# Performance work log

Measured on AMD Instinct MI355X. Metric: run time of the kernel, lower is better.

Reference implementation:

```python
import jax, jax.numpy as jnp
import numpy as np

N, H, E, P = 100000, 64, 1600000, 3


def setup_inputs() -> dict:
    key = jax.random.key(0)
    ks = jax.random.split(key, 12)
    h = jax.random.normal(ks[0], (N, H), dtype=jnp.float32)
    W = jax.random.normal(ks[1], (P, H, H), dtype=jnp.float32) * 0.1
    b = jnp.zeros((P, H), dtype=jnp.float32)
    a = jnp.full((P,), 0.25, dtype=jnp.float32)  # PReLU slopes (torch default init)
    fc_w = jax.random.normal(ks[2], (H, H), dtype=jnp.float32) * 0.1
    fc_b = jnp.zeros((H,), dtype=jnp.float32)
    att = jax.random.normal(ks[3], (H,), dtype=jnp.float32) * 0.1
    adj_vals = jax.random.uniform(ks[4], (E,), dtype=jnp.float32) * (1.0 / 16.0)
    row = jax.random.randint(ks[5], (E,), 0, N, dtype=jnp.int32)
    col = jax.random.randint(ks[6], (E,), 0, N, dtype=jnp.int32)
    mask1 = jax.random.randint(ks[7], (N,), 0, 2, dtype=jnp.int32).astype(bool)
    mask2 = jax.random.randint(ks[8], (N,), 0, 2, dtype=jnp.int32).astype(bool)
    return {"h": h, "W": W, "b": b, "a": a, "fc_w": fc_w, "fc_b": fc_b,
            "att": att, "adj_vals": adj_vals, "row": row, "col": col,
            "mask1": mask1, "mask2": mask2}


def reference(h, W, b, a, fc_w, fc_b, att, adj_vals, row, col, mask1, mask2):
    n = h.shape[0]

    def gcn_all(x):
        # P GCN layers (small fixed P): linear -> spmm(adj) -> +bias -> PReLU
        outs = []
        for p in range(W.shape[0]):
            fts = x @ W[p].T                                   # [N,H]
            msg = fts[col] * adj_vals[:, None]                  # [E,H] gather
            agg = jax.ops.segment_sum(msg, row, num_segments=n) # [N,H] scatter-add
            o = agg + b[p]
            outs.append(jnp.where(o > 0, o, a[p] * o))          # PReLU
        return jnp.stack(outs)                                  # [P,N,H]

    def attention(embeds):
        # sp_p = mean_n tanh(fc(embed_p)); beta = softmax_p(att . sp_p)
        s = jnp.tanh(jnp.einsum('pnh,kh->pnk', embeds, fc_w) + fc_b).mean(axis=1)  # [P,H]
        beta = jax.nn.softmax(s @ att, axis=0)                                      # [P]
        return jnp.einsum('pnh,p->nh', embeds, beta)                                # [N,H]

    h_masked = h * (~mask1)[:, None].astype(h.dtype)
    z_mp = attention(gcn_all(h_masked))       # encode with mask_ratio1
    z_mp2 = attention(gcn_all(h))             # encode with mask_ratio 0
    z_masked = z_mp * (~mask2)[:, None].astype(h.dtype)
    x_recon = attention(gcn_all(z_masked))    # decode
    return (z_mp, z_mp2, x_recon)
```

## Files before the change

kernel.cpp:

```cpp
#include <hip/hip_runtime.h>
#include <hip/hip_bf16.h>

typedef __hip_bfloat16 bf16;
typedef __attribute__((ext_vector_type(8))) short bf16x8;
typedef __attribute__((ext_vector_type(4))) float f32x4;


__device__ __forceinline__ short f2bf(float x) {
    unsigned u = __float_as_uint(x);
    unsigned r = (u + 0x7FFFu + ((u >> 16) & 1u)) >> 16;
    return (short)r;
}
__device__ __forceinline__ float bf2f(short s) {
    return __uint_as_float(((unsigned)(unsigned short)s) << 16);
}
__device__ __forceinline__ void split1(float v, short& h, short& l) {
    h = f2bf(v);
    l = f2bf(v - bf2f(h));
}

__device__ __forceinline__ void split8(const float* __restrict__ p, bool ok, bf16x8& hi,
                                       bf16x8& lo) {
    float v[8];
    if (ok) {
        float4 x0 = ((const float4*)p)[0];
        float4 x1 = ((const float4*)p)[1];
        v[0] = x0.x; v[1] = x0.y; v[2] = x0.z; v[3] = x0.w;
        v[4] = x1.x; v[5] = x1.y; v[6] = x1.z; v[7] = x1.w;
    } else {
#pragma unroll
        for (int j = 0; j < 8; j++) v[j] = 0.f;
    }
#pragma unroll
    for (int j = 0; j < 8; j++) {
        short hb = f2bf(v[j]);
        hi[j] = hb;
        lo[j] = f2bf(v[j] - bf2f(hb));
    }
}

__device__ __forceinline__ float fast_tanh(float x) {
    x = fminf(fmaxf(x, -15.f), 15.f);
    float t = __expf(2.f * x);
    return __fdividef(t - 1.f, t + 1.f);
}

__device__ __forceinline__ void fma4(float4& acc, float v, const float4& x) {
    acc.x = fmaf(v, x.x, acc.x);
    acc.y = fmaf(v, x.y, acc.y);
    acc.z = fmaf(v, x.z, acc.z);
    acc.w = fmaf(v, x.w, acc.w);
}

__device__ __forceinline__ void red4(float4& a) {
    a.x += __shfl_xor(a.x, 16); a.y += __shfl_xor(a.y, 16);
    a.z += __shfl_xor(a.z, 16); a.w += __shfl_xor(a.w, 16);
    a.x += __shfl_xor(a.x, 32); a.y += __shfl_xor(a.y, 32);
    a.z += __shfl_xor(a.z, 32); a.w += __shfl_xor(a.w, 32);
}

__global__ __launch_bounds__(256) void forensic_kernel(const unsigned int* __restrict__ mask_w,
                                                       const unsigned int* __restrict__ idx_w,
                                                       int nw_mask, int nw_idx,
                                                       int* __restrict__ flags) {
    __shared__ int sm[6];
    int t = threadIdx.x;
    if (t < 6) sm[t] = 0;
    __syncthreads();
    int m_gt1 = 0, m_f32 = 0, m_f64 = 0, m_oddnz = 0, i_hi = 0, i_oddnz = 0;
    for (int i = t; i < nw_mask; i += 256) {
        unsigned int w = mask_w[i];
        if (w > 1u && w != 0x3F800000u && w != 0x3FF00000u) m_gt1++;
        if (w == 0x3F800000u) m_f32++;
        if ((i & 1) && w == 0x3FF00000u) m_f64++;
        if ((i & 1) && w != 0u) m_oddnz++;
    }
    for (int i = t; i < nw_idx; i += 256) {
        unsigned int v = idx_w[i];
        if (v >= 0x20000000u) i_hi++;
        if ((i & 1) && v != 0u) i_oddnz++;
    }
    atomicAdd(&sm[0], m_gt1);
    atomicAdd(&sm[1], m_f32);
    atomicAdd(&sm[2], m_f64);
    atomicAdd(&sm[3], m_oddnz);
    atomicAdd(&sm[4], i_hi);
    atomicAdd(&sm[5], i_oddnz);
    __syncthreads();
    if (t == 0) {
        int mmode;
        if (sm[1] > 50) mmode = 2;
        else if (sm[2] > 50) mmode = 4;
        else if (sm[0] > 50) mmode = 0;
        else if (sm[3] > 50) mmode = 1;
        else mmode = 3;
        int imode;
        if (sm[4] > (nw_idx * 3) / 4) imode = 2;
        else if (sm[4] > nw_idx / 4) imode = 4;
        else if (sm[5] > 50) imode = 1;
        else imode = 3;
        flags[0] = mmode;
        flags[1] = imode;
    }
}

__device__ __forceinline__ int fetch_idx(const void* p, int e, int mode) {
    switch (mode) {
        case 1: return ((const int*)p)[e];
        case 3: return (int)(((const long long*)p)[e]);
        case 2: return (int)(((const float*)p)[e]);
        default: return (int)(((const double*)p)[e]);
    }
}

__device__ __forceinline__ bool conv_one(const void* m, int mode, int i) {
    switch (mode) {
        case 0: return ((const unsigned char*)m)[i] != 0;
        case 1: return ((const int*)m)[i] != 0;
        case 2: return ((const float*)m)[i] != 0.f;
        case 3: return ((const long long*)m)[i] != 0;
        default: return ((const double*)m)[i] != 0.0;
    }
}

__global__ __launch_bounds__(256) void conv_masks(const void* __restrict__ m1,
                                                  const void* __restrict__ m2,
                                                  const int* __restrict__ flags, int n,
                                                  unsigned char* __restrict__ o1,
                                                  unsigned char* __restrict__ o2) {
    int mode = flags[0];
    int i = blockIdx.x * 256 + threadIdx.x;
    if (i >= n) return;
    o1[i] = conv_one(m1, mode, i) ? 1 : 0;
    o2[i] = conv_one(m2, mode, i) ? 1 : 0;
}


__global__ __launch_bounds__(256) void bucket_hist(const void* __restrict__ row,
                                                   const int* __restrict__ flags, int e_cnt,
                                                   int n, int shift, int nb,
                                                   int* __restrict__ bcnt) {
    __shared__ int hist[2048];
    int t = threadIdx.x;
    for (int i = t; i < nb; i += 256) hist[i] = 0;
    __syncthreads();
    int imode = flags[1];
    for (int e = blockIdx.x * 256 + t; e < e_cnt; e += gridDim.x * 256) {
        int r = fetch_idx(row, e, imode);
        if ((unsigned)r < (unsigned)n) atomicAdd(&hist[r >> shift], 1);
    }
    __syncthreads();
    for (int i = t; i < nb; i += 256)
        if (hist[i]) atomicAdd(&bcnt[i], hist[i]);
}

__global__ __launch_bounds__(1024) void bucket_scan(int* __restrict__ bptr, int nb,
                                                    int* __restrict__ bcur, int n,
                                                    int* __restrict__ row_ptr) {
    __shared__ int sh[1024];
    int t = threadIdx.x;
    int i0 = t * 2, i1 = t * 2 + 1;
    int a = (i0 < nb) ? bptr[i0] : 0;
    int b = (i1 < nb) ? bptr[i1] : 0;
    int s = a + b;
    sh[t] = s;
    __syncthreads();
    for (int off = 1; off < 1024; off <<= 1) {
        int u = (t >= off) ? sh[t - off] : 0;
        __syncthreads();
        sh[t] += u;
        __syncthreads();
    }
    int base = sh[t] - s;
    if (i0 < nb) { bptr[i0] = base; bcur[i0] = base; }
    if (i1 < nb) { bptr[i1] = base + a; bcur[i1] = base + a; }
    if (t == 1023) {
        bptr[nb] = sh[1023];
        row_ptr[n] = sh[1023];
    }
}

__global__ __launch_bounds__(256) void bin_pass2(const void* __restrict__ row,
                                                 const void* __restrict__ col,
                                                 const float* __restrict__ vals,
                                                 const int* __restrict__ flags, int e_cnt, int n,
                                                 int shift, int nb, int* __restrict__ bcur,
                                                 int2* __restrict__ rcbin,
                                                 float* __restrict__ valbin) {
    __shared__ int hist[2048];
    __shared__ int base[2048];
    int t = threadIdx.x;
    int e0 = blockIdx.x * 2048;
    if (e0 >= e_cnt) return;
    int imode = flags[1];
    for (int i = t; i < nb; i += 256) hist[i] = 0;
    __syncthreads();
    int rr[8], cc[8];
    float vv[8];
    bool ok[8];
#pragma unroll
    for (int j = 0; j < 8; j++) {
        int e = e0 + j * 256 + t;
        ok[j] = false;
        if (e < e_cnt) {
            int r = fetch_idx(row, e, imode);
            if ((unsigned)r < (unsigned)n) {
                ok[j] = true;
                rr[j] = r;
                int c = fetch_idx(col, e, imode);
                cc[j] = ((unsigned)c < (unsigned)n) ? c : 0;
                vv[j] = vals[e];
                atomicAdd(&hist[r >> shift], 1);
            }
        }
    }
    __syncthreads();
    for (int i = t; i < nb; i += 256) {
        int c = hist[i];
        base[i] = c ? atomicAdd(&bcur[i], c) : 0;
        hist[i] = 0;
    }
    __syncthreads();
#pragma unroll
    for (int j = 0; j < 8; j++) {
        if (ok[j]) {
            int bk = rr[j] >> shift;
            int pos = base[bk] + atomicAdd(&hist[bk], 1);
            rcbin[pos] = make_int2(rr[j], cc[j]);
            valbin[pos] = vv[j];
        }
    }
}

__global__ __launch_bounds__(512) void csr_finalize(const int* __restrict__ bptr,
                                                    const int2* __restrict__ rcbin,
                                                    const float* __restrict__ valbin, int n,
                                                    int shift, int* __restrict__ row_ptr,
                                                    int* __restrict__ col_s,
                                                    float* __restrict__ val_s) {
    __shared__ int cnt[1024];
    __shared__ int curs[1024];
    __shared__ int red[512];
    int b = blockIdx.x, t = threadIdx.x;
    int rpb = 1 << shift;
    int r0 = b << shift;
    int rows = n - r0;
    if (rows <= 0) return;
    if (rows > rpb) rows = rpb;
    int ebase = bptr[b], eend = bptr[b + 1];
    for (int i = t; i < rows; i += 512) cnt[i] = 0;
    __syncthreads();
    for (int e = ebase + t; e < eend; e += 512) atomicAdd(&cnt[rcbin[e].x - r0], 1);
    __syncthreads();
    int v[2], s = 0;
#pragma unroll
    for (int j = 0; j < 2; j++) {
        int idx = t * 2 + j;
        v[j] = (idx < rows) ? cnt[idx] : 0;
        s += v[j];
    }
    red[t] = s;
    __syncthreads();
    for (int off = 1; off < 512; off <<= 1) {
        int u = (t >= off) ? red[t - off] : 0;
        __syncthreads();
        red[t] += u;
        __syncthreads();
    }
    int run = ebase + red[t] - s;
#pragma unroll
    for (int j = 0; j < 2; j++) {
        int idx = t * 2 + j;
        if (idx < rows) {
            row_ptr[r0 + idx] = run;
            curs[idx] = run;
            run += v[j];
        }
    }
    __syncthreads();
    for (int e = ebase + t; e < eend; e += 512) {
        int2 rc = rcbin[e];
        float vv = valbin[e];
        int pos = atomicAdd(&curs[rc.x - r0], 1);
        col_s[pos] = rc.y;
        val_s[pos] = vv;
    }
}


__device__ __forceinline__ void store_split4(short* __restrict__ hi, short* __restrict__ lo,
                                             size_t o, const float4& v) {
    short4 h4, l4;
    split1(v.x, h4.x, l4.x); split1(v.y, h4.y, l4.y);
    split1(v.z, h4.z, l4.z); split1(v.w, h4.w, l4.w);
    *(short4*)(hi + o) = h4;
    *(short4*)(lo + o) = l4;
}

__global__ __launch_bounds__(256) void spmm_dual(const float* __restrict__ X,
                                                 const int* __restrict__ row_ptr,
                                                 const int* __restrict__ col_s,
                                                 const float* __restrict__ val_s,
                                                 const unsigned char* __restrict__ mask, int n,
                                                 short* __restrict__ axm_hi,
                                                 short* __restrict__ axm_lo,
                                                 short* __restrict__ axf_hi,
                                                 short* __restrict__ axf_lo) {
    int gid = blockIdx.x * 256 + threadIdx.x;
    int r = gid >> 6;
    if (r >= n) return;
    int lane = threadIdx.x & 63;
    int g = lane >> 4, sub = lane & 15;
    int s = row_ptr[r], e = row_ptr[r + 1];
    int cnt = e - s;
    int myc = 0;
    float myvf = 0.f, myvm = 0.f;
    if (lane < cnt) {
        myc = col_s[s + lane];
        float v = val_s[s + lane];
        myvf = v;
        myvm = mask[myc] ? 0.f : v;
    }
    int cmain = cnt > 64 ? 64 : cnt;
    float4 fA = {0, 0, 0, 0}, fB = {0, 0, 0, 0}, mA = {0, 0, 0, 0}, mB = {0, 0, 0, 0};
    for (int i = 0; i < cmain; i += 16) {
        int i0 = i + g, i1 = i + 4 + g, i2 = i + 8 + g, i3 = i + 12 + g;
        int c0 = __shfl(myc, i0), c1 = __shfl(myc, i1);
        int c2 = __shfl(myc, i2), c3 = __shfl(myc, i3);
        float vf0 = __shfl(myvf, i0), vf1 = __shfl(myvf, i1);
        float vf2 = __shfl(myvf, i2), vf3 = __shfl(myvf, i3);
        float vm0 = __shfl(myvm, i0), vm1 = __shfl(myvm, i1);
        float vm2 = __shfl(myvm, i2), vm3 = __shfl(myvm, i3);
        if (i0 < cmain) {
            float4 x = *(const float4*)(X + (size_t)c0 * 64 + sub * 4);
            fma4(fA, vf0, x);
            fma4(mA, vm0, x);
        }
        if (i1 < cmain) {
            float4 x = *(const float4*)(X + (size_t)c1 * 64 + sub * 4);
            fma4(fB, vf1, x);
            fma4(mB, vm1, x);
        }
        if (i2 < cmain) {
            float4 x = *(const float4*)(X + (size_t)c2 * 64 + sub * 4);
            fma4(fA, vf2, x);
            fma4(mA, vm2, x);
        }
        if (i3 < cmain) {
            float4 x = *(const float4*)(X + (size_t)c3 * 64 + sub * 4);
            fma4(fB, vf3, x);
            fma4(mB, vm3, x);
        }
    }
    for (int i = 64 + g; i < cnt; i += 4) {
        int c = col_s[s + i];
        float v = val_s[s + i];
        float vm = mask[c] ? 0.f : v;
        float4 x = *(const float4*)(X + (size_t)c * 64 + sub * 4);
        fma4(fA, v, x);
        fma4(mA, vm, x);
    }
    fA.x += fB.x; fA.y += fB.y; fA.z += fB.z; fA.w += fB.w;
    mA.x += mB.x; mA.y += mB.y; mA.z += mB.z; mA.w += mB.w;
    red4(fA);
    red4(mA);
    if (g == 0) {
        size_t o = (size_t)r * 64 + sub * 4;
        store_split4(axf_hi, axf_lo, o, fA);
        store_split4(axm_hi, axm_lo, o, mA);
    }
}

__global__ __launch_bounds__(256) void spmm_one(const float* __restrict__ X,
                                                const int* __restrict__ row_ptr,
                                                const int* __restrict__ col_s,
                                                const float* __restrict__ val_s,
                                                const unsigned char* __restrict__ mask, int n,
                                                short* __restrict__ ax_hi,
                                                short* __restrict__ ax_lo) {
    int gid = blockIdx.x * 256 + threadIdx.x;
    int r = gid >> 6;
    if (r >= n) return;
    int lane = threadIdx.x & 63;
    int g = lane >> 4, sub = lane & 15;
    int s = row_ptr[r], e = row_ptr[r + 1];
    int cnt = e - s;
    int myc = 0;
    float myv = 0.f;
    if (lane < cnt) {
        myc = col_s[s + lane];
        float v = val_s[s + lane];
        myv = mask[myc] ? 0.f : v;
    }
    int cmain = cnt > 64 ? 64 : cnt;
    float4 aA = {0, 0, 0, 0}, aB = {0, 0, 0, 0};
    for (int i = 0; i < cmain; i += 16) {
        int i0 = i + g, i1 = i + 4 + g, i2 = i + 8 + g, i3 = i + 12 + g;
        int c0 = __shfl(myc, i0), c1 = __shfl(myc, i1);
        int c2 = __shfl(myc, i2), c3 = __shfl(myc, i3);
        float v0 = __shfl(myv, i0), v1 = __shfl(myv, i1);
        float v2 = __shfl(myv, i2), v3 = __shfl(myv, i3);
        if (i0 < cmain && v0 != 0.f) {
            float4 x = *(const float4*)(X + (size_t)c0 * 64 + sub * 4);
            fma4(aA, v0, x);
        }
        if (i1 < cmain && v1 != 0.f) {
            float4 x = *(const float4*)(X + (size_t)c1 * 64 + sub * 4);
            fma4(aB, v1, x);
        }
        if (i2 < cmain && v2 != 0.f) {
            float4 x = *(const float4*)(X + (size_t)c2 * 64 + sub * 4);
            fma4(aA, v2, x);
        }
        if (i3 < cmain && v3 != 0.f) {
            float4 x = *(const float4*)(X + (size_t)c3 * 64 + sub * 4);
            fma4(aB, v3, x);
        }
    }
    for (int i = 64 + g; i < cnt; i += 4) {
        int c = col_s[s + i];
        if (mask[c]) continue;
        float v = val_s[s + i];
        float4 x = *(const float4*)(X + (size_t)c * 64 + sub * 4);
        fma4(aA, v, x);
    }
    aA.x += aB.x; aA.y += aB.y; aA.z += aB.z; aA.w += aB.w;
    red4(aA);
    if (g == 0) {
        size_t o = (size_t)r * 64 + sub * 4;
        store_split4(ax_hi, ax_lo, o, aA);
    }
}


template <int PP>
__global__ __launch_bounds__(256) void gemm_tanh(const short* __restrict__ Xhi0,
                                                 const short* __restrict__ Xlo0,
                                                 const short* __restrict__ Xhi1,
                                                 const short* __restrict__ Xlo1,
                                                 const float* __restrict__ Wg,
                                                 const float* __restrict__ b,
                                                 const float* __restrict__ a,
                                                 const float* __restrict__ fcw,
                                                 const float* __restrict__ fcb, int n, int ntiles,
                                                 float* __restrict__ s_sums) {
    __shared__ __align__(16) short ehi[PP][16][72], elo[PP][16][72];
    int set = blockIdx.y;
    const short* __restrict__ Xhi = set ? Xhi1 : Xhi0;
    const short* __restrict__ Xlo = set ? Xlo1 : Xlo0;
    float* __restrict__ ss = s_sums + set * 512;
    int t = threadIdx.x;
    int wv = t >> 6, lane = t & 63, nl = lane & 15, q = lane >> 4;
    int colg = wv * 16 + nl;
    bf16x8 whi[PP][2], wlo[PP][2];
    float bias[PP], slope[PP];
#pragma unroll
    for (int p = 0; p < PP; p++) {
#pragma unroll
        for (int kk = 0; kk < 2; kk++)
            split8(Wg + p * 4096 + colg * 64 + kk * 32 + q * 8, true, whi[p][kk], wlo[p][kk]);
        bias[p] = b[p * 64 + colg];
        slope[p] = a[p];
    }
    bf16x8 fhi[2], flo[2];
#pragma unroll
    for (int kk = 0; kk < 2; kk++)
        split8(fcw + colg * 64 + kk * 32 + q * 8, true, fhi[kk], flo[kk]);
    float fbias = fcb[colg];
    float ssum[PP];
#pragma unroll
    for (int p = 0; p < PP; p++) ssum[p] = 0.f;

    int rt = blockIdx.x;
    bf16x8 ah[2], al[2];
    if (rt < ntiles) {
        size_t rb = (size_t)(rt * 16 + nl) * 64 + q * 8;
#pragma unroll
        for (int kk = 0; kk < 2; kk++) {
            ah[kk] = *(const bf16x8*)(Xhi + rb + kk * 32);
            al[kk] = *(const bf16x8*)(Xlo + rb + kk * 32);
        }
    }
    for (; rt < ntiles; rt += gridDim.x) {
#pragma unroll
        for (int p = 0; p < PP; p++) {
            f32x4 acc = {0.f, 0.f, 0.f, 0.f};
            acc = __builtin_amdgcn_mfma_f32_16x16x32_bf16(ah[0], whi[p][0], acc, 0, 0, 0);
            acc = __builtin_amdgcn_mfma_f32_16x16x32_bf16(ah[1], whi[p][1], acc, 0, 0, 0);
            acc = __builtin_amdgcn_mfma_f32_16x16x32_bf16(al[0], whi[p][0], acc, 0, 0, 0);
            acc = __builtin_amdgcn_mfma_f32_16x16x32_bf16(al[1], whi[p][1], acc, 0, 0, 0);
            acc = __builtin_amdgcn_mfma_f32_16x16x32_bf16(ah[0], wlo[p][0], acc, 0, 0, 0);
            acc = __builtin_amdgcn_mfma_f32_16x16x32_bf16(ah[1], wlo[p][1], acc, 0, 0, 0);
            acc = __builtin_amdgcn_mfma_f32_16x16x32_bf16(al[0], wlo[p][0], acc, 0, 0, 0);
            acc = __builtin_amdgcn_mfma_f32_16x16x32_bf16(al[1], wlo[p][1], acc, 0, 0, 0);
#pragma unroll
            for (int i = 0; i < 4; i++) {
                float o = acc[i] + bias[p];
                o = (o > 0.f) ? o : slope[p] * o;
                short hb, lb;
                split1(o, hb, lb);
                ehi[p][q * 4 + i][colg] = hb;
                elo[p][q * 4 + i][colg] = lb;
            }
        }
        int rn = rt + gridDim.x;
        bf16x8 pfh[2], pfl[2];
        if (rn < ntiles) {
            size_t rb = (size_t)(rn * 16 + nl) * 64 + q * 8;
#pragma unroll
            for (int kk = 0; kk < 2; kk++) {
                pfh[kk] = *(const bf16x8*)(Xhi + rb + kk * 32);
                pfl[kk] = *(const bf16x8*)(Xlo + rb + kk * 32);
            }
        }
        __syncthreads();
#pragma unroll
        for (int p = 0; p < PP; p++) {
            bf16x8 eh[2], el[2];
#pragma unroll
            for (int kk = 0; kk < 2; kk++) {
                eh[kk] = *(const bf16x8*)(&ehi[p][nl][kk * 32 + q * 8]);
                el[kk] = *(const bf16x8*)(&elo[p][nl][kk * 32 + q * 8]);
            }
            f32x4 acc = {0.f, 0.f, 0.f, 0.f};
            acc = __builtin_amdgcn_mfma_f32_16x16x32_bf16(eh[0], fhi[0], acc, 0, 0, 0);
            acc = __builtin_amdgcn_mfma_f32_16x16x32_bf16(eh[1], fhi[1], acc, 0, 0, 0);
            acc = __builtin_amdgcn_mfma_f32_16x16x32_bf16(el[0], fhi[0], acc, 0, 0, 0);
            acc = __builtin_amdgcn_mfma_f32_16x16x32_bf16(el[1], fhi[1], acc, 0, 0, 0);
            acc = __builtin_amdgcn_mfma_f32_16x16x32_bf16(eh[0], flo[0], acc, 0, 0, 0);
            acc = __builtin_amdgcn_mfma_f32_16x16x32_bf16(eh[1], flo[1], acc, 0, 0, 0);
#pragma unroll
            for (int i = 0; i < 4; i++) {
                int r = rt * 16 + q * 4 + i;
                if (r < n) ssum[p] += fast_tanh(acc[i] + fbias);
            }
        }
        __syncthreads();
#pragma unroll
        for (int kk = 0; kk < 2; kk++) {
            ah[kk] = pfh[kk];
            al[kk] = pfl[kk];
        }
    }
#pragma unroll
    for (int p = 0; p < PP; p++) {
        float s = ssum[p];
        s += __shfl_xor(s, 16);
        s += __shfl_xor(s, 32);
        if (q == 0) atomicAdd(&ss[p * 64 + colg], s);
    }
}


template <int PP>
__global__ __launch_bounds__(256) void gemm_mix(const short* __restrict__ Xhi0,
                                                const short* __restrict__ Xlo0,
                                                const short* __restrict__ Xhi1,
                                                const short* __restrict__ Xlo1,
                                                const float* __restrict__ Wg,
                                                const float* __restrict__ b,
                                                const float* __restrict__ a,
                                                const float* __restrict__ beta, int n, int ntiles,
                                                float* __restrict__ outbase, int accum) {
    int set = blockIdx.y;
    const short* __restrict__ Xhi = set ? Xhi1 : Xhi0;
    const short* __restrict__ Xlo = set ? Xlo1 : Xlo0;
    float* __restrict__ out = outbase + (size_t)set * n * 64;
    int t = threadIdx.x;
    int wv = t >> 6, lane = t & 63, nl = lane & 15, q = lane >> 4;
    int colg = wv * 16 + nl;
    bf16x8 whi[PP][2], wlo[PP][2];
    float bias[PP], slope[PP], bet[PP];
#pragma unroll
    for (int p = 0; p < PP; p++) {
#pragma unroll
        for (int kk = 0; kk < 2; kk++)
            split8(Wg + p * 4096 + colg * 64 + kk * 32 + q * 8, true, whi[p][kk], wlo[p][kk]);
        bias[p] = b[p * 64 + colg];
        slope[p] = a[p];
        bet[p] = beta[set * 8 + p];
    }
    int rt = blockIdx.x;
    bf16x8 ah[2], al[2];
    if (rt < ntiles) {
        size_t rb = (size_t)(rt * 16 + nl) * 64 + q * 8;
#pragma unroll
        for (int kk = 0; kk < 2; kk++) {
            ah[kk] = *(const bf16x8*)(Xhi + rb + kk * 32);
            al[kk] = *(const bf16x8*)(Xlo + rb + kk * 32);
        }
    }
    for (; rt < ntiles; rt += gridDim.x) {
        int rn = rt + gridDim.x;
        bf16x8 pfh[2], pfl[2];
        if (rn < ntiles) {
            size_t rb = (size_t)(rn * 16 + nl) * 64 + q * 8;
#pragma unroll
            for (int kk = 0; kk < 2; kk++) {
                pfh[kk] = *(const bf16x8*)(Xhi + rb + kk * 32);
                pfl[kk] = *(const bf16x8*)(Xlo + rb + kk * 32);
            }
        }
        float mix[4] = {0.f, 0.f, 0.f, 0.f};
#pragma unroll
        for (int p = 0; p < PP; p++) {
            f32x4 acc = {0.f, 0.f, 0.f, 0.f};
            acc = __builtin_amdgcn_mfma_f32_16x16x32_bf16(ah[0], whi[p][0], acc, 0, 0, 0);
            acc = __builtin_amdgcn_mfma_f32_16x16x32_bf16(ah[1], whi[p][1], acc, 0, 0, 0);
            acc = __builtin_amdgcn_mfma_f32_16x16x32_bf16(al[0], whi[p][0], acc, 0, 0, 0);
            acc = __builtin_amdgcn_mfma_f32_16x16x32_bf16(al[1], whi[p][1], acc, 0, 0, 0);
            acc = __builtin_amdgcn_mfma_f32_16x16x32_bf16(ah[0], wlo[p][0], acc, 0, 0, 0);
            acc = __builtin_amdgcn_mfma_f32_16x16x32_bf16(ah[1], wlo[p][1], acc, 0, 0, 0);
            acc = __builtin_amdgcn_mfma_f32_16x16x32_bf16(al[0], wlo[p][0], acc, 0, 0, 0);
            acc = __builtin_amdgcn_mfma_f32_16x16x32_bf16(al[1], wlo[p][1], acc, 0, 0, 0);
#pragma unroll
            for (int i = 0; i < 4; i++) {
                float o = acc[i] + bias[p];
                o = (o > 0.f) ? o : slope[p] * o;
                mix[i] = fmaf(bet[p], o, mix[i]);
            }
        }
#pragma unroll
        for (int i = 0; i < 4; i++) {
            int r = rt * 16 + q * 4 + i;
            if (r < n) {
                size_t idx = (size_t)r * 64 + colg;
                out[idx] = accum ? (out[idx] + mix[i]) : mix[i];
            }
        }
#pragma unroll
        for (int kk = 0; kk < 2; kk++) {
            ah[kk] = pfh[kk];
            al[kk] = pfl[kk];
        }
    }
}

__global__ __launch_bounds__(64) void compute_beta(const float* __restrict__ s_sums,
                                                   const float* __restrict__ att, int n, int P,
                                                   int nsets, float* __restrict__ beta) {
    int lane = threadIdx.x;
    float av = att[lane];
    for (int st = 0; st < nsets; st++) {
        const float* ss = s_sums + st * 512;
        float l[8];
        for (int p = 0; p < P; p++) l[p] = ss[p * 64 + lane] * av;
#pragma unroll
        for (int off = 32; off > 0; off >>= 1)
            for (int p = 0; p < 8; p++)
                if (p < P) l[p] += __shfl_down(l[p], off);
        if (lane == 0) {
            const float inv = 1.0f / (float)n;
            float m = -1e30f;
            for (int p = 0; p < P; p++) {
                l[p] *= inv;
                m = fmaxf(m, l[p]);
            }
            float s = 0.f;
            for (int p = 0; p < P; p++) {
                l[p] = __expf(l[p] - m);
                s += l[p];
            }
            for (int p = 0; p < P; p++) beta[st * 8 + p] = l[p] / s;
        }
    }
}


extern "C" void kernel_launch(void* const* d_in, const int* in_sizes, int n_in,
                              void* d_out, int out_size, void* d_ws, size_t ws_size,
                              hipStream_t stream) {
    const float* h = (const float*)d_in[0];
    const float* W = (const float*)d_in[1];
    const float* b = (const float*)d_in[2];
    const float* a = (const float*)d_in[3];
    const float* fc_w = (const float*)d_in[4];
    const float* fc_b = (const float*)d_in[5];
    const float* att = (const float*)d_in[6];
    const float* adj = (const float*)d_in[7];
    const void* row = d_in[8];
    const void* col = d_in[9];
    const void* mask1 = d_in[10];
    const void* mask2 = d_in[11];
    float* out = (float*)d_out;

    int P = in_sizes[3];
    if (P < 1 || P > 8) P = 3;
    int N = in_sizes[0] / 64;
    int E = in_sizes[7];
    int N16 = (N + 15) & ~15;
    int ntiles = N16 >> 4;

    int shift = 8;
    while (((N >> shift) + 1) > 2048) shift++;
    int NB = (N >> shift) + 1;

    char* w = (char*)d_ws;
    auto alloc = [&](size_t bytes) {
        void* p = (void*)w;
        w += (bytes + 255) & ~(size_t)255;
        return p;
    };
    int* row_ptr = (int*)alloc((size_t)(N + 1) * 4);
    int* col_s = (int*)alloc((size_t)E * 4);
    float* val_s = (float*)alloc((size_t)E * 4);
    int* bptr = (int*)alloc((size_t)(NB + 1) * 4);
    int* bcur = (int*)alloc((size_t)NB * 4);
    int2* rcbin = (int2*)alloc((size_t)E * 8);
    float* valbin = (float*)alloc((size_t)E * 4);
    unsigned char* m1c = (unsigned char*)alloc(N);
    unsigned char* m2c = (unsigned char*)alloc(N);
    short* axm_hi = (short*)alloc((size_t)N16 * 64 * 2);
    short* axm_lo = (short*)alloc((size_t)N16 * 64 * 2);
    short* axf_hi = (short*)alloc((size_t)N16 * 64 * 2);
    short* axf_lo = (short*)alloc((size_t)N16 * 64 * 2);
    float* s_sums = (float*)alloc(2 * 512 * 4);
    float* beta = (float*)alloc(64 * 4);
    int* flags = (int*)alloc(256);

    int nw_mask = N / 4 > 25000 ? 25000 : N / 4;
    int nw_idx = E / 4 > 25000 ? 25000 : E / 4;
    forensic_kernel<<<1, 256, 0, stream>>>((const unsigned int*)mask1, (const unsigned int*)row,
                                           nw_mask, nw_idx, flags);
    conv_masks<<<(N + 255) / 256, 256, 0, stream>>>(mask1, mask2, flags, N, m1c, m2c);

    hipMemsetAsync(bptr, 0, (size_t)(NB + 1) * 4, stream);
    if (N16 > N) {
        size_t padoff = (size_t)N * 64, padbytes = (size_t)(N16 - N) * 64 * 2;
        hipMemsetAsync(axm_hi + padoff, 0, padbytes, stream);
        hipMemsetAsync(axm_lo + padoff, 0, padbytes, stream);
        hipMemsetAsync(axf_hi + padoff, 0, padbytes, stream);
        hipMemsetAsync(axf_lo + padoff, 0, padbytes, stream);
    }
    bucket_hist<<<1024, 256, 0, stream>>>(row, flags, E, N, shift, NB, bptr);
    bucket_scan<<<1, 1024, 0, stream>>>(bptr, NB, bcur, N, row_ptr);
    int bin_blocks = (E + 2047) / 2048;
    bin_pass2<<<bin_blocks, 256, 0, stream>>>(row, col, adj, flags, E, N, shift, NB, bcur, rcbin,
                                              valbin);
    csr_finalize<<<NB, 512, 0, stream>>>(bptr, rcbin, valbin, N, shift, row_ptr, col_s, val_s);

    int spmm_grid = (int)(((size_t)N * 64 + 255) / 256);
    int tanh_blocks = 1024;
    int mix_blocks = 1024;

    auto tail = [&](const short* xh0, const short* xl0, const short* xh1, const short* xl1,
                    int nsets, float* dst) {
        hipMemsetAsync(s_sums, 0, 2 * 512 * 4, stream);
        if (P == 3) {
            gemm_tanh<3><<<dim3(tanh_blocks, nsets), 256, 0, stream>>>(
                xh0, xl0, xh1, xl1, W, b, a, fc_w, fc_b, N, ntiles, s_sums);
        } else {
            for (int p = 0; p < P; p++)
                gemm_tanh<1><<<dim3(tanh_blocks, nsets), 256, 0, stream>>>(
                    xh0, xl0, xh1, xl1, W + p * 4096, b + p * 64, a + p, fc_w, fc_b, N, ntiles,
                    s_sums + p * 64);
        }
        compute_beta<<<1, 64, 0, stream>>>(s_sums, att, N, P, nsets, beta);
        if (P == 3) {
            gemm_mix<3><<<dim3(mix_blocks, nsets), 256, 0, stream>>>(
                xh0, xl0, xh1, xl1, W, b, a, beta, N, ntiles, dst, 0);
        } else {
            for (int p = 0; p < P; p++)
                gemm_mix<1><<<dim3(mix_blocks, nsets), 256, 0, stream>>>(
                    xh0, xl0, xh1, xl1, W + p * 4096, b + p * 64, a + p, beta + p, N, ntiles, dst,
                    p != 0);
        }
    };

    spmm_dual<<<spmm_grid, 256, 0, stream>>>(h, row_ptr, col_s, val_s, m1c, N, axm_hi, axm_lo,
                                             axf_hi, axf_lo);
    tail(axm_hi, axm_lo, axf_hi, axf_lo, 2, out);
    spmm_one<<<spmm_grid, 256, 0, stream>>>(out, row_ptr, col_s, val_s, m2c, N, axm_hi, axm_lo);
    tail(axm_hi, axm_lo, axm_hi, axm_lo, 1, out + (size_t)2 * N * 64);
}
```

Baseline: 561.4 us.

## Presplit weights once, cheapen tanh and bf16 split, derive masked spmm by subtraction

Adds a one-time kernel that splits W and fc_w into bf16 hi/lo pairs, so the GEMM blocks no longer redo that split in their prologue. The hi part of the activation split now uses truncation instead of rounding, and tanh drops its clamp and uses a 1-2/(t+1) form. In spmm_dual the mask bit is packed into the column index, only masked-out contributions are accumulated, and the masked sum is taken as full minus that, which cuts FMAs and shuffles. The subtraction and the clampless tanh can change numerics slightly (cancellation, and exp overflow relying on inf handling).

```diff
diff --git a/kernel.cpp b/kernel.cpp
--- a/kernel.cpp
+++ b/kernel.cpp
@@ -17,6 +17,12 @@
 __device__ __forceinline__ void split1(float v, short& h, short& l) {
     h = f2bf(v);
     l = f2bf(v - bf2f(h));
+}
+__device__ __forceinline__ void split1_rtz(float v, short& h, short& l) {
+    unsigned u = __float_as_uint(v);
+    h = (short)(u >> 16);
+    float r = v - __uint_as_float(u & 0xFFFF0000u);
+    l = f2bf(r);
 }
 
 __device__ __forceinline__ void split8(const float* __restrict__ p, bool ok, bf16x8& hi,
@@ -40,9 +46,8 @@
 }
 
 __device__ __forceinline__ float fast_tanh(float x) {
-    x = fminf(fmaxf(x, -15.f), 15.f);
-    float t = __expf(2.f * x);
-    return __fdividef(t - 1.f, t + 1.f);
+    float t = __expf(x + x);
+    return 1.f - __fdividef(2.f, t + 1.f);
 }
 
 __device__ __forceinline__ void fma4(float4& acc, float v, const float4& x) {
@@ -133,6 +138,28 @@
     if (i >= n) return;
     o1[i] = conv_one(m1, mode, i) ? 1 : 0;
     o2[i] = conv_one(m2, mode, i) ? 1 : 0;
+}
+
+
+__global__ __launch_bounds__(256) void split_weights(const float* __restrict__ W,
+                                                     const float* __restrict__ fcw, int wn,
+                                                     int fn, short* __restrict__ whi,
+                                                     short* __restrict__ wlo,
+                                                     short* __restrict__ fhi,
+                                                     short* __restrict__ flo) {
+    int i = blockIdx.x * 256 + threadIdx.x;
+    if (i < wn) {
+        short h, l;
+        split1(W[i], h, l);
+        whi[i] = h;
+        wlo[i] = l;
+    } else if (i < wn + fn) {
+        int j = i - wn;
+        short h, l;
+        split1(fcw[j], h, l);
+        fhi[j] = h;
+        flo[j] = l;
+    }
 }
 
 
@@ -313,58 +340,56 @@
     int g = lane >> 4, sub = lane & 15;
     int s = row_ptr[r], e = row_ptr[r + 1];
     int cnt = e - s;
-    int myc = 0;
-    float myvf = 0.f, myvm = 0.f;
+    int mycm = 0;
+    float myv = 0.f;
     if (lane < cnt) {
-        myc = col_s[s + lane];
-        float v = val_s[s + lane];
-        myvf = v;
-        myvm = mask[myc] ? 0.f : v;
+        int c = col_s[s + lane];
+        myv = val_s[s + lane];
+        mycm = c | (mask[c] ? (1 << 30) : 0);
     }
     int cmain = cnt > 64 ? 64 : cnt;
-    float4 fA = {0, 0, 0, 0}, fB = {0, 0, 0, 0}, mA = {0, 0, 0, 0}, mB = {0, 0, 0, 0};
+    float4 fA = {0, 0, 0, 0}, fB = {0, 0, 0, 0};
+    float4 dA = {0, 0, 0, 0}, dB = {0, 0, 0, 0};
     for (int i = 0; i < cmain; i += 16) {
         int i0 = i + g, i1 = i + 4 + g, i2 = i + 8 + g, i3 = i + 12 + g;
-        int c0 = __shfl(myc, i0), c1 = __shfl(myc, i1);
-        int c2 = __shfl(myc, i2), c3 = __shfl(myc, i3);
-        float vf0 = __shfl(myvf, i0), vf1 = __shfl(myvf, i1);
-        float vf2 = __shfl(myvf, i2), vf3 = __shfl(myvf, i3);
-        float vm0 = __shfl(myvm, i0), vm1 = __shfl(myvm, i1);
-        float vm2 = __shfl(myvm, i2), vm3 = __shfl(myvm, i3);
+        int c0 = __shfl(mycm, i0), c1 = __shfl(mycm, i1);
+        int c2 = __shfl(mycm, i2), c3 = __shfl(mycm, i3);
+        float v0 = __shfl(myv, i0), v1 = __shfl(myv, i1);
+        float v2 = __shfl(myv, i2), v3 = __shfl(myv, i3);
         if (i0 < cmain) {
-            float4 x = *(const float4*)(X + (size_t)c0 * 64 + sub * 4);
-            fma4(fA, vf0, x);
-            fma4(mA, vm0, x);
+            float4 x = *(const float4*)(X + (size_t)(c0 & 0x3FFFFFFF) * 64 + sub * 4);
+            fma4(fA, v0, x);
+            if (c0 >> 30) fma4(dA, v0, x);
         }
         if (i1 < cmain) {
-            float4 x = *(const float4*)(X + (size_t)c1 * 64 + sub * 4);
-            fma4(fB, vf1, x);
-            fma4(mB, vm1, x);
+            float4 x = *(const float4*)(X + (size_t)(c1 & 0x3FFFFFFF) * 64 + sub * 4);
+            fma4(fB, v1, x);
+            if (c1 >> 30) fma4(dB, v1, x);
         }
         if (i2 < cmain) {
-            float4 x = *(const float4*)(X + (size_t)c2 * 64 + sub * 4);
-            fma4(fA, vf2, x);
-            fma4(mA, vm2, x);
+            float4 x = *(const float4*)(X + (size_t)(c2 & 0x3FFFFFFF) * 64 + sub * 4);
+            fma4(fA, v2, x);
+            if (c2 >> 30) fma4(dA, v2, x);
         }
         if (i3 < cmain) {
-            float4 x = *(const float4*)(X + (size_t)c3 * 64 + sub * 4);
-            fma4(fB, vf3, x);
-            fma4(mB, vm3, x);
+            float4 x = *(const float4*)(X + (size_t)(c3 & 0x3FFFFFFF) * 64 + sub * 4);
+            fma4(fB, v3, x);
+            if (c3 >> 30) fma4(dB, v3, x);
         }
     }
     for (int i = 64 + g; i < cnt; i += 4) {
         int c = col_s[s + i];
         float v = val_s[s + i];
-        float vm = mask[c] ? 0.f : v;
         float4 x = *(const float4*)(X + (size_t)c * 64 + sub * 4);
         fma4(fA, v, x);
-        fma4(mA, vm, x);
+        if (mask[c]) fma4(dA, v, x);
     }
     fA.x += fB.x; fA.y += fB.y; fA.z += fB.z; fA.w += fB.w;
-    mA.x += mB.x; mA.y += mB.y; mA.z += mB.z; mA.w += mB.w;
+    dA.x += dB.x; dA.y += dB.y; dA.z += dB.z; dA.w += dB.w;
     red4(fA);
-    red4(mA);
+    red4(dA);
     if (g == 0) {
+        float4 mA = make_float4(fA.x - dA.x, fA.y - dA.y, fA.z - dA.z, fA.w - dA.w);
         size_t o = (size_t)r * 64 + sub * 4;
         store_split4(axf_hi, axf_lo, o, fA);
         store_split4(axm_hi, axm_lo, o, mA);
@@ -438,10 +463,12 @@
                                                  const short* __restrict__ Xlo0,
                                                  const short* __restrict__ Xhi1,
                                                  const short* __restrict__ Xlo1,
-                                                 const float* __restrict__ Wg,
+                                                 const short* __restrict__ Whi_g,
+                                                 const short* __restrict__ Wlo_g,
                                                  const float* __restrict__ b,
                                                  const float* __restrict__ a,
-                                                 const float* __restrict__ fcw,
+                                                 const short* __restrict__ fchi_g,
+                                                 const short* __restrict__ fclo_g,
                                                  const float* __restrict__ fcb, int n, int ntiles,
                                                  float* __restrict__ s_sums) {
     __shared__ __align__(16) short ehi[PP][16][72], elo[PP][16][72];
@@ -457,15 +484,19 @@
 #pragma unroll
     for (int p = 0; p < PP; p++) {
 #pragma unroll
-        for (int kk = 0; kk < 2; kk++)
-            split8(Wg + p * 4096 + colg * 64 + kk * 32 + q * 8, true, whi[p][kk], wlo[p][kk]);
+        for (int kk = 0; kk < 2; kk++) {
+            whi[p][kk] = *(const bf16x8*)(Whi_g + p * 4096 + colg * 64 + kk * 32 + q * 8);
+            wlo[p][kk] = *(const bf16x8*)(Wlo_g + p * 4096 + colg * 64 + kk * 32 + q * 8);
+        }
         bias[p] = b[p * 64 + colg];
         slope[p] = a[p];
     }
     bf16x8 fhi[2], flo[2];
 #pragma unroll
-    for (int kk = 0; kk < 2; kk++)
-        split8(fcw + colg * 64 + kk * 32 + q * 8, true, fhi[kk], flo[kk]);
+    for (int kk = 0; kk < 2; kk++) {
+        fhi[kk] = *(const bf16x8*)(fchi_g + colg * 64 + kk * 32 + q * 8);
+        flo[kk] = *(const bf16x8*)(fclo_g + colg * 64 + kk * 32 + q * 8);
+    }
     float fbias = fcb[colg];
     float ssum[PP];
 #pragma unroll
@@ -498,7 +529,7 @@
                 float o = acc[i] + bias[p];
                 o = (o > 0.f) ? o : slope[p] * o;
                 short hb, lb;
-                split1(o, hb, lb);
+                split1_rtz(o, hb, lb);
                 ehi[p][q * 4 + i][colg] = hb;
                 elo[p][q * 4 + i][colg] = lb;
             }
@@ -557,7 +588,8 @@
                                                 const short* __restrict__ Xlo0,
                                                 const short* __restrict__ Xhi1,
                                                 const short* __restrict__ Xlo1,
-                                                const float* __restrict__ Wg,
+                                                const short* __restrict__ Whi_g,
+                                                const short* __restrict__ Wlo_g,
                                                 const float* __restrict__ b,
                                                 const float* __restrict__ a,
                                                 const float* __restrict__ beta, int n, int ntiles,
@@ -574,8 +606,10 @@
 #pragma unroll
     for (int p = 0; p < PP; p++) {
 #pragma unroll
-        for (int kk = 0; kk < 2; kk++)
-            split8(Wg + p * 4096 + colg * 64 + kk * 32 + q * 8, true, whi[p][kk], wlo[p][kk]);
+        for (int kk = 0; kk < 2; kk++) {
+            whi[p][kk] = *(const bf16x8*)(Whi_g + p * 4096 + colg * 64 + kk * 32 + q * 8);
+            wlo[p][kk] = *(const bf16x8*)(Wlo_g + p * 4096 + colg * 64 + kk * 32 + q * 8);
+        }
         bias[p] = b[p * 64 + colg];
         slope[p] = a[p];
         bet[p] = beta[set * 8 + p];
@@ -714,6 +748,10 @@
     short* axm_lo = (short*)alloc((size_t)N16 * 64 * 2);
     short* axf_hi = (short*)alloc((size_t)N16 * 64 * 2);
     short* axf_lo = (short*)alloc((size_t)N16 * 64 * 2);
+    short* whi_g = (short*)alloc((size_t)8 * 4096 * 2);
+    short* wlo_g = (short*)alloc((size_t)8 * 4096 * 2);
+    short* fchi_g = (short*)alloc((size_t)4096 * 2);
+    short* fclo_g = (short*)alloc((size_t)4096 * 2);
     float* s_sums = (float*)alloc(2 * 512 * 4);
     float* beta = (float*)alloc(64 * 4);
     int* flags = (int*)alloc(256);
@@ -723,6 +761,9 @@
     forensic_kernel<<<1, 256, 0, stream>>>((const unsigned int*)mask1, (const unsigned int*)row,
                                            nw_mask, nw_idx, flags);
     conv_masks<<<(N + 255) / 256, 256, 0, stream>>>(mask1, mask2, flags, N, m1c, m2c);
+    int wn = P * 4096, fn = 4096;
+    split_weights<<<(wn + fn + 255) / 256, 256, 0, stream>>>(W, fc_w, wn, fn, whi_g, wlo_g,
+                                                            fchi_g, fclo_g);
 
     hipMemsetAsync(bptr, 0, (size_t)(NB + 1) * 4, stream);
     if (N16 > N) {
@@ -748,22 +789,22 @@
         hipMemsetAsync(s_sums, 0, 2 * 512 * 4, stream);
         if (P == 3) {
             gemm_tanh<3><<<dim3(tanh_blocks, nsets), 256, 0, stream>>>(
-                xh0, xl0, xh1, xl1, W, b, a, fc_w, fc_b, N, ntiles, s_sums);
+                xh0, xl0, xh1, xl1, whi_g, wlo_g, b, a, fchi_g, fclo_g, fc_b, N, ntiles, s_sums);
         } else {
             for (int p = 0; p < P; p++)
                 gemm_tanh<1><<<dim3(tanh_blocks, nsets), 256, 0, stream>>>(
-                    xh0, xl0, xh1, xl1, W + p * 4096, b + p * 64, a + p, fc_w, fc_b, N, ntiles,
-                    s_sums + p * 64);
+                    xh0, xl0, xh1, xl1, whi_g + p * 4096, wlo_g + p * 4096, b + p * 64, a + p,
+                    fchi_g, fclo_g, fc_b, N, ntiles, s_sums + p * 64);
         }
         compute_beta<<<1, 64, 0, stream>>>(s_sums, att, N, P, nsets, beta);
         if (P == 3) {
             gemm_mix<3><<<dim3(mix_blocks, nsets), 256, 0, stream>>>(
-                xh0, xl0, xh1, xl1, W, b, a, beta, N, ntiles, dst, 0);
+                xh0, xl0, xh1, xl1, whi_g, wlo_g, b, a, beta, N, ntiles, dst, 0);
         } else {
             for (int p = 0; p < P; p++)
                 gemm_mix<1><<<dim3(mix_blocks, nsets), 256, 0, stream>>>(
-                    xh0, xl0, xh1, xl1, W + p * 4096, b + p * 64, a + p, beta + p, N, ntiles, dst,
-                    p != 0);
+                    xh0, xl0, xh1, xl1, whi_g + p * 4096, wlo_g + p * 4096, b + p * 64, a + p,
+                    beta + p, N, ntiles, dst, p != 0);
         }
     };
 
```

After: 568.1 us. No clear change (+1.2%).
